# Performance work log

Hardware: AMD Instinct MI355X
Metric: run time of the kernel (lower is better)

## Reference

```python
import jax, jax.numpy as jnp
import numpy as np

DIM = 192; NH = 6; WS = 8; SS = 4
D_INNER = 384; D_STATE = 64; MNH = 6; HEADDIM = 64; DCONV = 4; CHUNK = 128


def layernorm(x, w, b):
    m = jnp.mean(x, axis=-1, keepdims=True)
    v = jnp.var(x, axis=-1, keepdims=True)
    return (x - m) * jax.lax.rsqrt(v + 1e-5) * w + b


def segsum(a):
    # a: (..., T) -> (..., T, T) with [i,j] = sum_{k=j+1..i} a_k (lower-tri), -inf-ish above diag
    T = a.shape[-1]
    x = jnp.broadcast_to(a[..., None], a.shape + (T,))
    lo = np.tril(np.ones((T, T), dtype=bool), -1)
    x = jnp.where(lo, x, 0.0)
    s = jnp.cumsum(x, axis=-2)
    keep = np.tril(np.ones((T, T), dtype=bool), 0)
    return jnp.where(keep, s, -1e9)


def ssd(X, a, Bm, Cm):
    # Mamba2 chunked state-space dual scan. X:(b,l,h,p) a:(b,l,h) Bm/Cm:(b,l,n)
    b, l, h, p = X.shape
    n = Bm.shape[-1]
    nc = l // CHUNK
    Xc = X.reshape(b, nc, CHUNK, h, p)
    ac = a.reshape(b, nc, CHUNK, h).transpose(0, 3, 1, 2)  # (b,h,c,cl)
    Bc = Bm.reshape(b, nc, CHUNK, n)
    Cc = Cm.reshape(b, nc, CHUNK, n)
    a_cs = jnp.cumsum(ac, axis=-1)
    Lm = jnp.exp(segsum(ac))  # (b,h,c,cl,cl)
    Y_diag = jnp.einsum('bcln,bcsn,bhcls,bcshp->bclhp', Cc, Bc, Lm, Xc)
    decay_states = jnp.exp(a_cs[..., -1:] - a_cs)
    states = jnp.einsum('bcln,bhcl,bclhp->bchpn', Bc, decay_states, Xc)
    a_last = jnp.pad(a_cs[..., -1], ((0, 0), (0, 0), (1, 0)))
    decay_chunk = jnp.exp(segsum(a_last))  # (b,h,c+1,c+1)
    states_cat = jnp.concatenate([jnp.zeros_like(states[:, :1]), states], axis=1)
    prev = jnp.einsum('bhzc,bchpn->bzhpn', decay_chunk, states_cat)[:, :-1]
    Y_off = jnp.einsum('bcln,bchpn,bhcl->bclhp', Cc, prev, jnp.exp(a_cs))
    return (Y_diag + Y_off).reshape(b, l, h, p)


def mamba2(xs, in_w, conv_w, conv_b, dt_bias, A_log, D, norm_w, out_w):
    b, l, _ = xs.shape
    zxbcdt = xs @ in_w.T  # (b,l,2*di+2*n+nh)
    z = zxbcdt[..., :D_INNER]
    xBC = zxbcdt[..., D_INNER:2 * D_INNER + 2 * D_STATE]
    dt = jax.nn.softplus(zxbcdt[..., -MNH:] + dt_bias)
    # causal depthwise conv1d
    xt = xBC.transpose(0, 2, 1)
    xt = jax.lax.conv_general_dilated(xt, conv_w[:, None, :], (1,), [(DCONV - 1, 0)],
                                      feature_group_count=xt.shape[1],
                                      dimension_numbers=('NCH', 'OIH', 'NCH'))
    xBC = jax.nn.silu((xt + conv_b[None, :, None]).transpose(0, 2, 1))
    xp = xBC[..., :D_INNER].reshape(b, l, MNH, HEADDIM)
    Bm = xBC[..., D_INNER:D_INNER + D_STATE]
    Cm = xBC[..., D_INNER + D_STATE:]
    A = -jnp.exp(A_log)
    y = ssd(xp * dt[..., None], dt * A, Bm, Cm)
    y = y + xp * D[None, None, :, None]
    y = y.reshape(b, l, D_INNER)
    y = y * jax.nn.silu(z)  # gated RMSNorm
    y = y * jax.lax.rsqrt(jnp.mean(y * y, axis=-1, keepdims=True) + 1e-5) * norm_w
    return y @ out_w.T


def build_mask(H, W):
    img = np.zeros((H, W))
    cnt = 0
    for hs in (slice(0, -WS), slice(-WS, -SS), slice(-SS, None)):
        for wsl in (slice(0, -WS), slice(-WS, -SS), slice(-SS, None)):
            img[hs, wsl] = cnt
            cnt += 1
    mw = img.reshape(H // WS, WS, W // WS, WS).transpose(0, 2, 1, 3).reshape(-1, WS * WS)
    diff = mw[:, None, :] - mw[:, :, None]
    return jnp.asarray(np.where(diff != 0, -100.0, 0.0).astype(np.float32))


def gated_window_attn(xw, mask, qkv_w, qkv_b, proj_w, proj_b, gate_w, gate_b):
    Bw, N, C = xw.shape
    hd = C // NH
    qkv = (xw @ qkv_w.T + qkv_b).reshape(Bw, N, 3, NH, hd).transpose(2, 0, 3, 1, 4)
    q, k, v = qkv[0], qkv[1], qkv[2]
    s = jnp.einsum('bhnd,bhmd->bhnm', q, k) * (hd ** -0.5)
    nW = mask.shape[0]
    s = (s.reshape(Bw // nW, nW, NH, N, N) + mask[None, :, None]).reshape(Bw, NH, N, N)
    a = jax.nn.softmax(s, axis=-1)
    o = jnp.einsum('bhnm,bhmd->bhnd', a, v).transpose(0, 2, 1, 3)  # (Bw,N,NH,hd)
    gate = jax.nn.sigmoid(xw @ gate_w.T + gate_b)  # per-head gate from pre-attn x
    o = (o * gate[..., None]).reshape(Bw, N, C)
    return o @ proj_w.T + proj_b


def lgs_forward(x, H, W, n1_w, n1_b, m_in_w, m_conv_w, m_conv_b, m_dt_bias, m_A_log,
                m_D, m_norm_w, m_out_w, qkv_w, qkv_b, proj_w, proj_b, gate_w, gate_b,
                fus_w, fus_b, eca_w, n2_w, n2_b, fc1_w, fc1_b, fc2_w, fc2_b):
    twoB, L, C = x.shape
    Bh = twoB // 2
    shortcut = x
    xn = layernorm(x, n1_w, n1_b)
    # Mamba branch: interleave frame0/frame1 tokens -> (Bh, 2L, C) scan -> de-interleave
    xs = jnp.stack([xn[:Bh], xn[Bh:]], axis=2).reshape(Bh, 2 * L, C)
    ym = mamba2(xs, m_in_w, m_conv_w, m_conv_b, m_dt_bias, m_A_log, m_D, m_norm_w, m_out_w)
    ym = ym.reshape(Bh, L, 2, C)
    x_mamba = jnp.concatenate([ym[:, :, 0], ym[:, :, 1]], axis=0)  # (2B,L,C)
    # shifted-window gated attention branch
    x2 = jnp.roll(xn.reshape(twoB, H, W, C), (-SS, -SS), axis=(1, 2))
    xw = x2.reshape(twoB, H // WS, WS, W // WS, WS, C).transpose(0, 1, 3, 2, 4, 5).reshape(-1, WS * WS, C)
    ow = gated_window_attn(xw, build_mask(H, W), qkv_w, qkv_b, proj_w, proj_b, gate_w, gate_b)
    ow = ow.reshape(twoB, H // WS, W // WS, WS, WS, C).transpose(0, 1, 3, 2, 4, 5).reshape(twoB, H, W, C)
    x_attn = jnp.roll(ow, (SS, SS), axis=(1, 2)).reshape(twoB, L, C)
    # fusion 1x1 conv == per-pixel linear over concatenated channels
    xf = jnp.concatenate([x_mamba, x_attn], axis=-1) @ fus_w.T + fus_b
    # ECAB: global-avg-pool channel attention via k=3 1D conv over channels
    pooled = jnp.pad(jnp.mean(xf, axis=1), ((0, 0), (1, 1)))
    ca = jax.nn.sigmoid(eca_w[0] * pooled[:, :-2] + eca_w[1] * pooled[:, 1:-1] + eca_w[2] * pooled[:, 2:])
    xf = xf * ca[:, None, :]
    xo = shortcut + xf
    h = layernorm(xo, n2_w, n2_b)
    h = jax.nn.gelu(h @ fc1_w.T + fc1_b, approximate=False) @ fc2_w.T + fc2_b
    return xo + h


def setup_inputs() -> dict:
    key = jax.random.key(0)
    ks = jax.random.split(key, 12)
    C = DIM

    def w(k, shape, s=0.02):
        return jax.random.normal(k, shape, jnp.float32) * s

    return {
        'x': jax.random.normal(ks[0], (4, 2304, C), jnp.float32),
        'H': 48, 'W': 48,
        'n1_w': jnp.ones((C,), jnp.float32), 'n1_b': jnp.zeros((C,), jnp.float32),
        'm_in_w': w(ks[1], (2 * D_INNER + 2 * D_STATE + MNH, C)),
        'm_conv_w': w(ks[2], (D_INNER + 2 * D_STATE, DCONV), 0.1),
        'm_conv_b': jnp.zeros((D_INNER + 2 * D_STATE,), jnp.float32),
        'm_dt_bias': jnp.log(jnp.expm1(jnp.full((MNH,), 0.01, jnp.float32))),
        'm_A_log': jnp.log(jnp.arange(1, MNH + 1, dtype=jnp.float32)),
        'm_D': jnp.ones((MNH,), jnp.float32),
        'm_norm_w': jnp.ones((D_INNER,), jnp.float32),
        'm_out_w': w(ks[3], (C, D_INNER)),
        'qkv_w': w(ks[4], (3 * C, C)), 'qkv_b': jnp.zeros((3 * C,), jnp.float32),
        'proj_w': w(ks[5], (C, C)), 'proj_b': jnp.zeros((C,), jnp.float32),
        'gate_w': w(ks[6], (NH, C)), 'gate_b': jnp.zeros((NH,), jnp.float32),
        'fus_w': w(ks[7], (C, 2 * C)), 'fus_b': jnp.zeros((C,), jnp.float32),
        'eca_w': w(ks[8], (3,), 0.3),
        'n2_w': jnp.ones((C,), jnp.float32), 'n2_b': jnp.zeros((C,), jnp.float32),
        'fc1_w': w(ks[9], (4 * C, C)), 'fc1_b': jnp.zeros((4 * C,), jnp.float32),
        'fc2_w': w(ks[10], (C, 4 * C)), 'fc2_b': jnp.zeros((C,), jnp.float32),
    }


def reference(x, H, W, n1_w, n1_b, m_in_w, m_conv_w, m_conv_b, m_dt_bias, m_A_log,
              m_D, m_norm_w, m_out_w, qkv_w, qkv_b, proj_w, proj_b, gate_w, gate_b,
              fus_w, fus_b, eca_w, n2_w, n2_b, fc1_w, fc1_b, fc2_w, fc2_b):
    return lgs_forward(x, H, W, n1_w, n1_b, m_in_w, m_conv_w, m_conv_b, m_dt_bias,
                       m_A_log, m_D, m_norm_w, m_out_w, qkv_w, qkv_b, proj_w, proj_b,
                       gate_w, gate_b, fus_w, fus_b, eca_w, n2_w, n2_b,
                       fc1_w, fc1_b, fc2_w, fc2_b)
```

## Files before the change

kernel.cpp:

```cpp
#include <hip/hip_runtime.h>
#include <math.h>

#define DEV __device__ __forceinline__

typedef __attribute__((ext_vector_type(8))) short short8;
typedef __attribute__((ext_vector_type(4))) float f32x4;

DEV float sigmoidf_(float x){ return 1.f/(1.f+__expf(-x)); }
DEV float siluf_(float x){ return x/(1.f+__expf(-x)); }
DEV float softplusf_(float x){ return (x>20.f)? x : log1pf(__expf(x)); }

DEV short bf16rne(float f){
  unsigned u=__float_as_uint(f);
  unsigned r=(u + 0x7FFFu + ((u>>16)&1u))>>16;
  return (short)r;
}
DEV unsigned short bf16u(float f){ return (unsigned short)bf16rne(f); }
DEV float b2f(unsigned short u){ return __uint_as_float(((unsigned)u)<<16); }
DEV float b2fs(short u){ return __uint_as_float(((unsigned)(unsigned short)u)<<16); }

DEV void gll16(const void* g, void* l){
  __builtin_amdgcn_global_load_lds(
      (const __attribute__((address_space(1))) void*)g,
      (__attribute__((address_space(3))) void*)(unsigned)(uintptr_t)l,
// ... 76 lines not shown
  #pragma unroll
  for(int p=0;p<NP;p++){
    if(p+1<NP) asm volatile("s_waitcnt vmcnt(4)":::"memory");
    else       asm volatile("s_waitcnt vmcnt(0)":::"memory");
    __builtin_amdgcn_s_barrier();
    compute(p,p&1);
    if(p+2<NP){
      __builtin_amdgcn_s_barrier();
      stage(p+2,p&1);
    }
  }

  __syncthreads();
  {
    int mbase=wid*16+4*kq;
    #pragma unroll
    for(int ni=0;ni<4;ni++)
      #pragma unroll
      for(int r=0;r<4;r++)
        sO[(mbase+r)*65 + ni*16+m16]=acc[ni][r];
  }
  __syncthreads();
  int erow=tid>>3, c0=(tid&7)*8;
  #pragma unroll
  for(int rd=0;rd<2;rd++){
    int ml=rd*32+erow;
    int m=bm+ml;
    int orow=map_row(m,smode);
    float v[8];
    #pragma unroll
    for(int j=0;j<8;j++) v[j]=sO[ml*65+c0+j];
    const float* rp=res? res+(size_t)orow*ldo+col_off : nullptr;
    #pragma unroll
    for(int j=0;j<8;j++){
      int nn=bn+c0+j;
      float val=v[j];
      if(bias && nn<N) val+=bias[nn];
      if(epi==2) val=0.5f*val*(1.f+erff(val*0.70710678118654752f));
      else if(epi==3) val+=rp[nn];
      v[j]=val;
    }
    size_t obase=(size_t)orow*ldo+col_off+bn+c0;
    if(bn+c0+7<N){
      if(Ob){
        short8 w;
        #pragma unroll
        for(int j=0;j<8;j++) w[j]=bf16rne(v[j]);
        *(short8*)(Ob+obase)=w;
      } else {
        float4 f0={v[0],v[1],v[2],v[3]}, f1={v[4],v[5],v[6],v[7]};
        *(float4*)(Of+obase)=f0;
        *(float4*)(Of+obase+4)=f1;
      }
    } else {
      #pragma unroll
      for(int j=0;j<8;j++){
        int nn=bn+c0+j;
        if(nn<N){ if(Ob) Ob[obase+j]=bf16rne(v[j]); else Of[obase+j]=v[j]; }
      }
    }
  }
  if(pool){
    if(tid<64){
      float s=0;
      #pragma unroll 8
      for(int ml=0;ml<64;ml++) s+=sO[ml*65+tid];
      if(bias) s+=64.f*bias[bn+tid];
      atomicAdd(&pool[(bm/2304)*192 + bn+tid], s);
    }
  }
}

template<int K>
__global__ __launch_bounds__(256,4) void k_gemm(const short* __restrict__ A, const short* __restrict__ W,
    const float* __restrict__ bias, const float* __restrict__ res,
    float* __restrict__ Of, short* __restrict__ Ob,
    int N, int ldo, int col_off, int gmode, int smode, int epi, float* __restrict__ pool){
  gemm_body<K>(A,W,bias,res,Of,Ob,N,ldo,col_off,gmode,smode,epi,blockIdx.x,blockIdx.y,pool);
}

__global__ __launch_bounds__(256,4) void k_gemm_inqkv(const short* __restrict__ xn,
    const short* __restrict__ w_in, short* __restrict__ zx,
    const short* __restrict__ w_qkv, const float* __restrict__ qkvb, short* __restrict__ qkv){
  if(blockIdx.y<15)
    gemm_body<192>(xn,w_in,nullptr,nullptr,nullptr,zx, 902,904,0, 1,0,0, blockIdx.x,blockIdx.y, nullptr);
  else
    gemm_body<192>(xn,w_qkv,qkvb,nullptr,nullptr,qkv, 576,576,0, 2,0,0, blockIdx.x,blockIdx.y-15, nullptr);
}

__global__ __launch_bounds__(256) void k_lnw2b(const float* __restrict__ in, const float* __restrict__ w,
    const float* __restrict__ b, short* __restrict__ out,
    const float* __restrict__ w0,const float* __restrict__ w1,const float* __restrict__ w2,
    const float* __restrict__ w3,const float* __restrict__ w4,const float* __restrict__ w5,
    const float* __restrict__ w6, short* __restrict__ dst){
  int bid=blockIdx.x;
  if(bid<2304){
    int warp=threadIdx.x>>6, lane=threadIdx.x&63;
    int row=bid*4+warp;
    const float* ip=in+(size_t)row*192;
    float v0=ip[lane], v1=ip[lane+64], v2=ip[lane+128];
    float s=v0+v1+v2, sq=v0*v0+v1*v1+v2*v2;
    #pragma unroll
    for(int off=32;off;off>>=1){ s+=__shfl_xor(s,off); sq+=__shfl_xor(sq,off); }
    float mean=s*(1.f/192.f), var=sq*(1.f/192.f)-mean*mean;
    float inv=rsqrtf(var+1e-5f);
    short* op=out+(size_t)row*192;
    op[lane]    =bf16rne((v0-mean)*inv*w[lane]    +b[lane]);
    op[lane+64] =bf16rne((v1-mean)*inv*w[lane+64] +b[lane+64]);
    op[lane+128]=bf16rne((v2-mean)*inv*w[lane+128]+b[lane+128]);
  } else {
    int flat=bid-2304;
    int seg=flat/677;
    int i=(flat-seg*677)*256+threadIdx.x;
    const float* src; int size, off;
    switch(seg){
      case 0: src=w0; size=173184; off=0;      break;
      case 1: src=w1; size=110592; off=173184; break;
      case 2: src=w2; size=73728;  off=283776; break;
      case 3: src=w3; size=36864;  off=357504; break;
      case 4: src=w4; size=73728;  off=394368; break;
      case 5: src=w5; size=147456; off=468096; break;
      default:src=w6; size=147456; off=615552; break;
    }
    if(i<size) dst[off+i]=bf16rne(src[i]);
  }
}

__global__ __launch_bounds__(256) void k_convprep(const short* __restrict__ zx, const float* __restrict__ cw,
    const float* __restrict__ cb, short* __restrict__ xbc,
    const float* __restrict__ dt_bias, const float* __restrict__ A_log,
    float* __restrict__ dtb, float* __restrict__ acs, float* __restrict__ csum){
  int bid=blockIdx.x;
  if(bid<2304){
    int idx=bid*256+threadIdx.x;
    int ch0=(idx&63)*8; int rl=idx>>6;
    int l=rl%4608;
    const short* base=zx+(size_t)rl*904+384+ch0;
    short8 x0=*(const short8*)(base);
    short8 x1={0,0,0,0,0,0,0,0},x2=x1,x3=x1;
    if(l>=1) x1=*(const short8*)(base-904);
    if(l>=2) x2=*(const short8*)(base-2*904);
    if(l>=3) x3=*(const short8*)(base-3*904);
    short8 out;
    #pragma unroll
    for(int j=0;j<8;j++){
      float4 w=*(const float4*)(cw+(ch0+j)*4);
      float acc=cb[ch0+j]
        + b2fs(x3[j])*w.x + b2fs(x2[j])*w.y + b2fs(x1[j])*w.z + b2fs(x0[j])*w.w;
      out[j]=bf16rne(siluf_(acc));
    }
    *(short8*)(xbc+(size_t)rl*512+ch0)=out;
  } else {
    int pb=bid-2304;
    int c=pb%36, h=(pb/36)%6, b=pb/216;
    int l=threadIdx.x;
    __shared__ float sb[128];
    float a=0.f;
    if(l<128){
      int row=b*4608+c*128+l;
      float xv=b2fs(zx[(size_t)row*904+896+h])+dt_bias[h];
      float dt=softplusf_(xv);
      a=-__expf(A_log[h])*dt;
      dtb[row*6+h]=dt;
      sb[l]=a;
    }
    __syncthreads();
    for(int off=1;off<128;off<<=1){
      float add=(l>=off && l<128)? sb[l-off]:0.f;
      __syncthreads();
      if(l<128) sb[l]+=add;
      __syncthreads();
    }
    if(l<128){
      acs[((size_t)(b*6+h)*36+c)*128+l]=sb[l];
      if(l==127) csum[(b*6+h)*36+c]=sb[127];
    }
  }
}

__global__ __launch_bounds__(256) void k_ssd_a(const short* __restrict__ xbc, const float* __restrict__ dtb,
    const float* __restrict__ acs, const float* __restrict__ csum,
    short* __restrict__ st, short* __restrict__ Y){
  int bid=blockIdx.x;
  int h=bid%6, c=(bid/6)%36, b=bid/216;
  __shared__ unsigned short sB[128][68];
  __shared__ unsigned short sC[128][68];
  __shared__ unsigned short sXdT[64][132];
  __shared__ unsigned short sBTE[64][132];
  __shared__ unsigned short sM[128][36];
  __shared__ float sAcs[128];
  __shared__ float sE[128];
  int tid=threadIdx.x;
  int lane=tid&63, wid=tid>>6;
  int m16=lane&15, kq=lane>>4;
  int base_row=b*4608+c*128;
  const float* acsp=acs+((size_t)(b*6+h)*36+c)*128;
  float tot=csum[(b*6+h)*36+c];
  if(tid<128){ float a=acsp[tid]; sAcs[tid]=a; sE[tid]=__expf(tot-a); }
  __syncthreads();
  for(int i=tid;i<1024;i+=256){
    int l=i>>3, n0=(i&7)*8;
    int row=base_row+l;
    const short* rp=xbc+(size_t)row*512;
    short8 Bv=*(const short8*)(rp+384+n0);
    short8 Cv=*(const short8*)(rp+448+n0);
    short8 Xv=*(const short8*)(rp+h*64+n0);
    float dt=dtb[row*6+h];
    float e=sE[l];
    *(short8*)&sB[l][n0]=Bv;
    *(short8*)&sC[l][n0]=Cv;
    #pragma unroll
    for(int j=0;j<8;j++){
      sXdT[n0+j][l]=bf16u(b2fs(Xv[j])*dt);
      sBTE[n0+j][l]=bf16u(b2fs(Bv[j])*e);
    }
  }
  __syncthreads();
  {
    int wr=wid>>1, wc=wid&1;
    f32x4 accS[2][2];
    #pragma unroll
    for(int mi=0;mi<2;mi++)
      #pragma unroll
      for(int ni=0;ni<2;ni++) accS[mi][ni]=(f32x4){0.f,0.f,0.f,0.f};
    #pragma unroll
    for(int ks=0;ks<4;ks++){
      short8 a0=*(const short8*)&sXdT[wr*32+m16][ks*32+kq*8];
      short8 a1=*(const short8*)&sXdT[wr*32+16+m16][ks*32+kq*8];
      short8 b0=*(const short8*)&sBTE[wc*32+m16][ks*32+kq*8];
      short8 b1=*(const short8*)&sBTE[wc*32+16+m16][ks*32+kq*8];
      accS[0][0]=__builtin_amdgcn_mfma_f32_16x16x32_bf16(a0,b0,accS[0][0],0,0,0);
      accS[0][1]=__builtin_amdgcn_mfma_f32_16x16x32_bf16(a0,b1,accS[0][1],0,0,0);
      accS[1][0]=__builtin_amdgcn_mfma_f32_16x16x32_bf16(a1,b0,accS[1][0],0,0,0);
      accS[1][1]=__builtin_amdgcn_mfma_f32_16x16x32_bf16(a1,b1,accS[1][1],0,0,0);
    }
    short* op=st+((size_t)((b*36+c)*6+h))*4096;
    #pragma unroll
    for(int mi=0;mi<2;mi++)
      #pragma unroll
      for(int ni=0;ni<2;ni++)
        #pragma unroll
        for(int r=0;r<4;r++){
          int p=wr*32+mi*16+4*kq+r, n=wc*32+ni*16+m16;
          op[p*64+n]=bf16rne(accS[mi][ni][r]);
        }
  }
  #pragma unroll
  for(int ti=0;ti<2;ti++){
    int t = ti? (7-wid) : wid;
    f32x4 accY[4];
    #pragma unroll
    for(int pi=0;pi<4;pi++) accY[pi]=(f32x4){0.f,0.f,0.f,0.f};
    int nslab=(t>>1)+1;
    for(int jt=0;jt<nslab;jt++){
      f32x4 accD[2];
      accD[0]=(f32x4){0.f,0.f,0.f,0.f}; accD[1]=(f32x4){0.f,0.f,0.f,0.f};
      #pragma unroll
      for(int ks=0;ks<2;ks++){
        short8 a =*(const short8*)&sC[t*16+m16][ks*32+kq*8];
        short8 b0=*(const short8*)&sB[jt*32+m16][ks*32+kq*8];
        short8 b1=*(const short8*)&sB[jt*32+16+m16][ks*32+kq*8];
        accD[0]=__builtin_amdgcn_mfma_f32_16x16x32_bf16(a,b0,accD[0],0,0,0);
        accD[1]=__builtin_amdgcn_mfma_f32_16x16x32_bf16(a,b1,accD[1],0,0,0);
      }
      int lrow=t*16+4*kq;
      #pragma unroll
      for(int sti=0;sti<2;sti++)
        #pragma unroll
        for(int r=0;r<4;r++){
          int l=lrow+r, s=jt*32+sti*16+m16;
          float v=(s<=l)? __expf(sAcs[l]-sAcs[s])*accD[sti][r] : 0.f;
          sM[l][sti*16+m16]=bf16u(v);
        }
      short8 am=*(const short8*)&sM[t*16+m16][kq*8];
      #pragma unroll
      for(int pi=0;pi<4;pi++){
        short8 bx=*(const short8*)&sXdT[pi*16+m16][jt*32+kq*8];
        accY[pi]=__builtin_amdgcn_mfma_f32_16x16x32_bf16(am,bx,accY[pi],0,0,0);
      }
    }
    #pragma unroll
    for(int pi=0;pi<4;pi++)
      #pragma unroll
      for(int r=0;r<4;r++){
        int l=t*16+4*kq+r, p=pi*16+m16;
        Y[(size_t)(base_row+l)*384+h*64+p]=bf16rne(accY[pi][r]);
      }
  }
}

__global__ __launch_bounds__(256) void k_scan(const short* __restrict__ st, const float* __restrict__ csum,
                                              short* __restrict__ prevb){
  int bid=blockIdx.x;
  int seg=bid&15, bh=bid>>4;
  int b=bh/6, h=bh%6;
  __shared__ float sE[36];
  if(threadIdx.x<36) sE[threadIdx.x]=__expf(csum[(b*6+h)*36+threadIdx.x]);
  __syncthreads();
  int e=seg*256+threadIdx.x;
  size_t stride=(size_t)6*4096;
  size_t idx=((size_t)((b*36+0)*6+h))*4096+e;
  float carry=0.f;
  for(int c4=0;c4<36;c4+=4){
    float v[4];
    #pragma unroll
    for(int j=0;j<4;j++) v[j]=b2fs(st[idx+j*stride]);
    #pragma unroll
    for(int j=0;j<4;j++){
      prevb[idx+j*stride]=bf16rne(carry);
      carry=carry*sE[c4+j]+v[j];
    }
    idx+=4*stride;
  }
}

__global__ __launch_bounds__(256) void k_ssd_b(const short* __restrict__ xbc, const short* __restrict__ prevb,
    const float* __restrict__ acs, const float* __restrict__ Dv, short* __restrict__ Y){
  int bid=blockIdx.x;
  int h=bid%6, c=(bid/6)%36, b=bid/216;
  __shared__ unsigned short sC[128][68];
  __shared__ unsigned short sP[64][68];
  __shared__ float sAcs[128];
  int tid=threadIdx.x;
  int lane=tid&63, wid=tid>>6;
  int m16=lane&15, kq=lane>>4;
  int base_row=b*4608+c*128;
  const float* acsp=acs+((size_t)(b*6+h)*36+c)*128;
  if(tid<128) sAcs[tid]=acsp[tid];
  for(int i=tid;i<1024;i+=256){
    int l=i>>3, n0=(i&7)*8;
    short8 Cv=*(const short8*)(xbc+(size_t)(base_row+l)*512+448+n0);
    *(short8*)&sC[l][n0]=Cv;
  }
  const short* pp=prevb+((size_t)((b*36+c)*6+h))*4096;
  for(int i=tid;i<512;i+=256){
    int p_=i>>3, n0=(i&7)*8;
    short8 Pv=*(const short8*)(pp+p_*64+n0);
    *(short8*)&sP[p_][n0]=Pv;
  }
  __syncthreads();
  float Dh=Dv[h];
  int lt0=2*wid;
  f32x4 acc[2][4];
  #pragma unroll
  for(int li=0;li<2;li++)
    #pragma unroll
    for(int pi=0;pi<4;pi++) acc[li][pi]=(f32x4){0.f,0.f,0.f,0.f};
  #pragma unroll
  for(int ks=0;ks<2;ks++){
    short8 a0=*(const short8*)&sC[lt0*16+m16][ks*32+kq*8];
    short8 a1=*(const short8*)&sC[(lt0+1)*16+m16][ks*32+kq*8];
    #pragma unroll
    for(int pi=0;pi<4;pi++){
      short8 bp=*(const short8*)&sP[pi*16+m16][ks*32+kq*8];
      acc[0][pi]=__builtin_amdgcn_mfma_f32_16x16x32_bf16(a0,bp,acc[0][pi],0,0,0);
      acc[1][pi]=__builtin_amdgcn_mfma_f32_16x16x32_bf16(a1,bp,acc[1][pi],0,0,0);
    }
  }
  #pragma unroll
  for(int li=0;li<2;li++){
    #pragma unroll
    for(int r=0;r<4;r++){
      int l=(lt0+li)*16+4*kq+r;
      int row=base_row+l;
      float e=__expf(sAcs[l]);
      #pragma unroll
      for(int pi=0;pi<4;pi++){
        int p=pi*16+m16;
        size_t yi=(size_t)row*384+h*64+p;
        float xpv=b2fs(xbc[(size_t)row*512+h*64+p]);
        Y[yi]=bf16rne(b2fs(Y[yi])+acc[li][pi][r]*e+xpv*Dh);
      }
    }
  }
}

__global__ __launch_bounds__(256) void k_rmsgate(const short* __restrict__ Y, const short* __restrict__ zx,
    const float* __restrict__ nw, short* __restrict__ yn, float* __restrict__ partial){
  if(blockIdx.x<3){
    int t=blockIdx.x*256+threadIdx.x;
    if(t<768) partial[t]=0.f;
  }
  int warp=threadIdx.x>>6, lane=threadIdx.x&63;
  int row=blockIdx.x*4+warp;
  float v[6]; float ss=0.f;
  #pragma unroll
  for(int j=0;j<6;j++){
    int cidx=lane+64*j;
    float y=b2fs(Y[(size_t)row*384+cidx]);
    float z=b2fs(zx[(size_t)row*904+cidx]);
    y*=siluf_(z);
    v[j]=y; ss+=y*y;
  }
  #pragma unroll
  for(int off=32;off;off>>=1) ss+=__shfl_xor(ss,off);
  float sc=rsqrtf(ss*(1.f/384.f)+1e-5f);
  #pragma unroll
  for(int j=0;j<6;j++){
    int cidx=lane+64*j;
    yn[(size_t)row*384+cidx]=bf16rne(v[j]*sc*nw[cidx]);
  }
}

__global__ __launch_bounds__(128) void k_att2(const short* __restrict__ qkv, const short* __restrict__ xn,
    const float* __restrict__ gw, const float* __restrict__ gb, short* __restrict__ obuf){
  int bid=blockIdx.x;
  int widx=bid/6, head=bid-widx*6;
  int b=widx/36, t=widx-b*36;
  int wi=t/6, wj=t-wi*6;
  int n=threadIdx.x&63, half=threadIdx.x>>6;
  __shared__ float sK[64][32], sV[64][32];
  __shared__ float sO2[64][32];
  __shared__ float sM2[64], sD2[64];
  const short* qp=qkv+(size_t)(widx*64+n)*576+head*32;
  float q[32];
  {
    short8 v0=*(const short8*)(qp),    v1=*(const short8*)(qp+8);
    short8 v2=*(const short8*)(qp+16), v3=*(const short8*)(qp+24);
    #pragma unroll
    for(int i=0;i<8;i++){ q[i]=b2fs(v0[i]); q[8+i]=b2fs(v1[i]); q[16+i]=b2fs(v2[i]); q[24+i]=b2fs(v3[i]); }
    short8 k0=*(const short8*)(qp+192+half*16), k1=*(const short8*)(qp+200+half*16);
    short8 u0=*(const short8*)(qp+384+half*16), u1=*(const short8*)(qp+392+half*16);
    #pragma unroll
    for(int i=0;i<8;i++){
      sK[n][half*16+i]=b2fs(k0[i]); sK[n][half*16+8+i]=b2fs(k1[i]);
      sV[n][half*16+i]=b2fs(u0[i]); sV[n][half*16+8+i]=b2fs(u1[i]);
    }
  }
  int h2=wi*8+(n>>3), w2=wj*8+(n&7);
  int rh=(h2<40)?0:((h2<44)?1:2);
  int rw=(w2<40)?0:((w2<44)?1:2);
  int myid=rh*3+rw;
  __syncthreads();
  const float scale=0.17677669529663687f;
  float p[32]; float mx=-1e30f;
  #pragma unroll 4
  for(int jj=0;jj<32;jj++){
    int j=half*32+jj;
    float sc=0;
    #pragma unroll
    for(int d=0;d<32;d++) sc+=q[d]*sK[j][d];
    int hj=wi*8+(j>>3), wjj=wj*8+(j&7);
    int rhj=(hj<40)?0:((hj<44)?1:2);
    int rwj=(wjj<40)?0:((wjj<44)?1:2);
    float m=((rhj*3+rwj)!=myid)? -100.f:0.f;
    float v=sc*scale+m;
    p[jj]=v; mx=fmaxf(mx,v);
  }
  float den=0;
  #pragma unroll
  for(int jj=0;jj<32;jj++){ p[jj]=__expf(p[jj]-mx); den+=p[jj]; }
  float o[32];
  #pragma unroll
  for(int d=0;d<32;d++) o[d]=0.f;
  #pragma unroll 4
  for(int jj=0;jj<32;jj++){
    float pj=p[jj];
    #pragma unroll
    for(int d=0;d<32;d++) o[d]+=pj*sV[half*32+jj][d];
  }
  if(half==1){
    sM2[n]=mx; sD2[n]=den;
    #pragma unroll
    for(int d=0;d<32;d++) sO2[n][d]=o[d];
  }
  __syncthreads();
  if(half==0){
    float m1=sM2[n], d1=sD2[n];
    float m=fmaxf(mx,m1);
    float e0=__expf(mx-m), e1=__expf(m1-m);
    float dent=den*e0+d1*e1;
    int xrow=map_row(widx*64+n,2);
    const short* xp=xn+(size_t)xrow*192;
    const float* gwp=gw+head*192;
    float g=0;
    #pragma unroll
    for(int c=0;c<24;c++){
      short8 xv=*(const short8*)(xp+c*8);
      float4 w0=*(const float4*)(gwp+c*8);
      float4 w1=*(const float4*)(gwp+c*8+4);
      g+=b2fs(xv[0])*w0.x+b2fs(xv[1])*w0.y+b2fs(xv[2])*w0.z+b2fs(xv[3])*w0.w
        +b2fs(xv[4])*w1.x+b2fs(xv[5])*w1.y+b2fs(xv[6])*w1.z+b2fs(xv[7])*w1.w;
    }
    g=sigmoidf_(g+gb[head]);
    float fac=g/dent;
    short* op=obuf+(size_t)(widx*64+n)*192+head*32;
    #pragma unroll
    for(int v8=0;v8<4;v8++){
      short8 w;
      #pragma unroll
      for(int j=0;j<8;j++){
        int d=v8*8+j;
        w[j]=bf16rne((o[d]*e0+sO2[n][d]*e1)*fac);
      }
      *(short8*)(op+v8*8)=w;
    }
  }
}

__global__ __launch_bounds__(768) void k_ca(const float* __restrict__ partial, const float* __restrict__ ecaw,
                                            float* __restrict__ ca){
  int tid=threadIdx.x;
  int cidx=tid%192;
  float pv=partial[tid]*(1.f/2304.f);
  __shared__ float sP[768];
  sP[tid]=pv; __syncthreads();
  float left =(cidx>0)?   sP[tid-1]:0.f;
  float right=(cidx<191)? sP[tid+1]:0.f;
  ca[tid]=sigmoidf_(ecaw[0]*left+ecaw[1]*pv+ecaw[2]*right);
}

__global__ __launch_bounds__(256) void k_xoln(const float* __restrict__ x, const float* __restrict__ xf,
    const float* __restrict__ ca, const float* __restrict__ w, const float* __restrict__ bvec,
    float* __restrict__ xo, short* __restrict__ out){
  int warp=threadIdx.x>>6, lane=threadIdx.x&63;
  int row=blockIdx.x*4+warp;
  int bidx=row/2304;
  const float* cap=ca+bidx*192;
  const float* xp=x+(size_t)row*192;
  const float* fp=xf+(size_t)row*192;
  float v0=xp[lane]    +fp[lane]    *cap[lane];
  float v1=xp[lane+64] +fp[lane+64] *cap[lane+64];
  float v2=xp[lane+128]+fp[lane+128]*cap[lane+128];
  float* op=xo+(size_t)row*192;
  op[lane]=v0; op[lane+64]=v1; op[lane+128]=v2;
  float s=v0+v1+v2, sq=v0*v0+v1*v1+v2*v2;
  #pragma unroll
  for(int off=32;off;off>>=1){ s+=__shfl_xor(s,off); sq+=__shfl_xor(sq,off); }
  float mean=s*(1.f/192.f), var=sq*(1.f/192.f)-mean*mean;
  float inv=rsqrtf(var+1e-5f);
  short* bp=out+(size_t)row*192;
  bp[lane]    =bf16rne((v0-mean)*inv*w[lane]    +bvec[lane]);
  bp[lane+64] =bf16rne((v1-mean)*inv*w[lane+64] +bvec[lane+64]);
  bp[lane+128]=bf16rne((v2-mean)*inv*w[lane+128]+bvec[lane+128]);
}

extern "C" void kernel_launch(void* const* d_in, const int* in_sizes, int n_in,
                              void* d_out, int out_size, void* d_ws, size_t ws_size,
                              hipStream_t stream){
  const float* x     =(const float*)d_in[0];
  const float* n1w   =(const float*)d_in[3];
  const float* n1b   =(const float*)d_in[4];
  const float* m_in_w=(const float*)d_in[5];
  const float* m_cw  =(const float*)d_in[6];
  const float* m_cb  =(const float*)d_in[7];
  const float* m_dtb =(const float*)d_in[8];
  const float* m_Al  =(const float*)d_in[9];
  const float* m_D   =(const float*)d_in[10];
  const float* m_nw  =(const float*)d_in[11];
  const float* m_ow  =(const float*)d_in[12];
  const float* qkvw  =(const float*)d_in[13];
  const float* qkvb  =(const float*)d_in[14];
  const float* projw =(const float*)d_in[15];
  const float* projb =(const float*)d_in[16];
  const float* gatew =(const float*)d_in[17];
  const float* gateb =(const float*)d_in[18];
  const float* fusw  =(const float*)d_in[19];
  const float* fusb  =(const float*)d_in[20];
  const float* ecaw  =(const float*)d_in[21];
  const float* n2w   =(const float*)d_in[22];
  const float* n2b   =(const float*)d_in[23];
  const float* fc1w  =(const float*)d_in[24];
  const float* fc1b  =(const float*)d_in[25];
  const float* fc2w  =(const float*)d_in[26];
  const float* fc2b  =(const float*)d_in[27];
  float* out=(float*)d_out;
  float* ws=(float*)d_ws;

  short* xn_bf  = (short*)(ws + 0);
  short* wb     = (short*)(ws + 884736);
  short* zx_bf  = (short*)(ws + 1266240);
  short* xbc_bf = (short*)(ws + 5431872);
  float* dtb    = ws + 7791168;
  float* acs    = ws + 7846464;
  float* csum   = ws + 7901760;
  short* st_bf  = (short*)(ws + 7902272);
  short* prevb_bf=(short*)(ws + 9671744);
  short* Y_bf   = (short*)(ws + 11441216);
  float* bigbf  = ws + 14980160;
  short* qkv_bf = (short*)(ws + 18519104);
  short* hbuf_bf= xn_bf;
  short* obuf_bf= xbc_bf;
  short* xcat_bf= prevb_bf;
  float* xf     = (float*)st_bf;
  float* xo     = (float*)Y_bf;
  short* yn_bf  = (short*)bigbf;
  short* h1_bf  = (short*)bigbf;
  float* partial= dtb;
  float* ca     = acs;
  short* wb_in  = wb + 0;
  short* wb_qkv = wb + 173184;
  short* wb_out = wb + 283776;
  short* wb_proj= wb + 357504;
  short* wb_fus = wb + 394368;
  short* wb_fc1 = wb + 468096;
  short* wb_fc2 = wb + 615552;

  k_lnw2b<<<7043,256,0,stream>>>(x,n1w,n1b,xn_bf, m_in_w,qkvw,m_ow,projw,fusw,fc1w,fc2w,wb);
  k_gemm_inqkv<<<dim3(144,24),256,0,stream>>>(xn_bf,wb_in,zx_bf,wb_qkv,qkvb,qkv_bf);
  k_convprep<<<2736,256,0,stream>>>(zx_bf,m_cw,m_cb,xbc_bf, m_dtb,m_Al,dtb,acs,csum);
  k_ssd_a<<<432,256,0,stream>>>(xbc_bf,dtb,acs,csum,st_bf,Y_bf);
  k_scan<<<192,256,0,stream>>>(st_bf,csum,prevb_bf);
  k_ssd_b<<<432,256,0,stream>>>(xbc_bf,prevb_bf,acs,m_D,Y_bf);
  k_rmsgate<<<2304,256,0,stream>>>(Y_bf,zx_bf,m_nw,yn_bf,partial);
  k_gemm<384><<<dim3(144,3),256,0,stream>>>(yn_bf,wb_out,nullptr,nullptr,nullptr,xcat_bf, 192,384,0, 0,1,0, nullptr);
  k_att2<<<864,128,0,stream>>>(qkv_bf,xn_bf,gatew,gateb,obuf_bf);
  k_gemm<192><<<dim3(144,3),256,0,stream>>>(obuf_bf,wb_proj,projb,nullptr,nullptr,xcat_bf, 192,384,192, 0,2,0, nullptr);
  k_gemm<384><<<dim3(144,3),256,0,stream>>>(xcat_bf,wb_fus,fusb,nullptr,xf,nullptr, 192,192,0, 0,0,0, partial);
  k_ca<<<1,768,0,stream>>>(partial,ecaw,ca);
  k_xoln<<<2304,256,0,stream>>>(x,xf,ca,n2w,n2b,xo,hbuf_bf);
  k_gemm<192><<<dim3(144,12),256,0,stream>>>(hbuf_bf,wb_fc1,fc1b,nullptr,nullptr,h1_bf, 768,768,0, 0,0,2, nullptr);
  k_gemm<768><<<dim3(144,3),256,0,stream>>>(h1_bf,wb_fc2,fc2b,xo,out,nullptr, 192,192,0, 0,0,3, nullptr);
}
```

Measured before the change: 170.7 us.

## Fuse window attention into SSD chunk kernel and fold channel attention into xoln

The window attention kernel becomes extra blocks of the SSD intra-chunk kernel, with a shared-memory union and two attention heads packed per 256-thread block. This lets the two independent stages run concurrently in one launch instead of in separate launches. The tiny single-block channel-attention kernel is removed and its sigmoid/conv is recomputed inline in the xoln kernel. The attention output gets its own workspace buffer so it no longer aliases the SSD input it now runs alongside. The costs are a larger union shared-memory footprint for the attention blocks and redundant per-row recomputation of the ECA gate.

After: 182.4 us. 6.9% more time.

```diff
diff --git a/kernel.cpp b/kernel.cpp
--- a/kernel.cpp
+++ b/kernel.cpp
@@ -182,10 +182,11 @@
 __global__ __launch_bounds__(256,4) void k_gemm_inqkv(const short* __restrict__ xn,
     const short* __restrict__ w_in, short* __restrict__ zx,
     const short* __restrict__ w_qkv, const float* __restrict__ qkvb, short* __restrict__ qkv){
-  if(blockIdx.y<15)
-    gemm_body<192>(xn,w_in,nullptr,nullptr,nullptr,zx, 902,904,0, 1,0,0, blockIdx.x,blockIdx.y, nullptr);
-  else
-    gemm_body<192>(xn,w_qkv,qkvb,nullptr,nullptr,qkv, 576,576,0, 2,0,0, blockIdx.x,blockIdx.y-15, nullptr);
+  int by=blockIdx.y;
+  const short* W; short* O; const float* bias; int N,ldo,gm,byy;
+  if(by<15){ W=w_in;  O=zx;  bias=nullptr; N=902; ldo=904; gm=1; byy=by; }
+  else     { W=w_qkv; O=qkv; bias=qkvb;    N=576; ldo=576; gm=2; byy=by-15; }
+  gemm_body<192>(xn,W,bias,nullptr,nullptr,O, N,ldo,0, gm,0,0, blockIdx.x,byy, nullptr);
 }
 
 __global__ __launch_bounds__(256) void k_lnw2b(const float* __restrict__ in, const float* __restrict__ w,
@@ -255,14 +256,12 @@
     int c=pb%36, h=(pb/36)%6, b=pb/216;
     int l=threadIdx.x;
     __shared__ float sb[128];
-    float a=0.f;
     if(l<128){
       int row=b*4608+c*128+l;
       float xv=b2fs(zx[(size_t)row*904+896+h])+dt_bias[h];
       float dt=softplusf_(xv);
-      a=-__expf(A_log[h])*dt;
       dtb[row*6+h]=dt;
-      sb[l]=a;
+      sb[l]=-__expf(A_log[h])*dt;
     }
     __syncthreads();
     for(int off=1;off<128;off<<=1){
@@ -278,114 +277,221 @@
   }
 }
 
-__global__ __launch_bounds__(256) void k_ssd_a(const short* __restrict__ xbc, const float* __restrict__ dtb,
+struct SsdS {
+  unsigned short sB[128][68];
+  unsigned short sC[128][68];
+  unsigned short sXdT[64][132];
+  unsigned short sBTE[64][132];
+  unsigned short sM[128][36];
+  float sAcs[128];
+  float sE[128];
+};
+struct AttS {
+  float sK[2][64][32];
+  float sV[2][64][32];
+  float sO2[2][64][32];
+  float sM2[2][64];
+  float sD2[2][64];
+};
+
+__global__ __launch_bounds__(256) void k_ssd_att(const short* __restrict__ xbc, const float* __restrict__ dtb,
     const float* __restrict__ acs, const float* __restrict__ csum,
-    short* __restrict__ st, short* __restrict__ Y){
-  int bid=blockIdx.x;
-  int h=bid%6, c=(bid/6)%36, b=bid/216;
-  __shared__ unsigned short sB[128][68];
-  __shared__ unsigned short sC[128][68];
-  __shared__ unsigned short sXdT[64][132];
-  __shared__ unsigned short sBTE[64][132];
-  __shared__ unsigned short sM[128][36];
-  __shared__ float sAcs[128];
-  __shared__ float sE[128];
+    short* __restrict__ st, short* __restrict__ Y,
+    const short* __restrict__ qkv, const short* __restrict__ xn,
+    const float* __restrict__ gw, const float* __restrict__ gb, short* __restrict__ obuf){
+  __shared__ union { SsdS s; AttS a; } u;
   int tid=threadIdx.x;
-  int lane=tid&63, wid=tid>>6;
-  int m16=lane&15, kq=lane>>4;
-  int base_row=b*4608+c*128;
-  const float* acsp=acs+((size_t)(b*6+h)*36+c)*128;
-  float tot=csum[(b*6+h)*36+c];
-  if(tid<128){ float a=acsp[tid]; sAcs[tid]=a; sE[tid]=__expf(tot-a); }
-  __syncthreads();
-  for(int i=tid;i<1024;i+=256){
-    int l=i>>3, n0=(i&7)*8;
-    int row=base_row+l;
-    const short* rp=xbc+(size_t)row*512;
-    short8 Bv=*(const short8*)(rp+384+n0);
-    short8 Cv=*(const short8*)(rp+448+n0);
-    short8 Xv=*(const short8*)(rp+h*64+n0);
-    float dt=dtb[row*6+h];
-    float e=sE[l];
-    *(short8*)&sB[l][n0]=Bv;
-    *(short8*)&sC[l][n0]=Cv;
-    #pragma unroll
-    for(int j=0;j<8;j++){
-      sXdT[n0+j][l]=bf16u(b2fs(Xv[j])*dt);
-      sBTE[n0+j][l]=bf16u(b2fs(Bv[j])*e);
-    }
-  }
-  __syncthreads();
-  {
-    int wr=wid>>1, wc=wid&1;
-    f32x4 accS[2][2];
-    #pragma unroll
-    for(int mi=0;mi<2;mi++)
-      #pragma unroll
-      for(int ni=0;ni<2;ni++) accS[mi][ni]=(f32x4){0.f,0.f,0.f,0.f};
-    #pragma unroll
-    for(int ks=0;ks<4;ks++){
-      short8 a0=*(const short8*)&sXdT[wr*32+m16][ks*32+kq*8];
-      short8 a1=*(const short8*)&sXdT[wr*32+16+m16][ks*32+kq*8];
-      short8 b0=*(const short8*)&sBTE[wc*32+m16][ks*32+kq*8];
-      short8 b1=*(const short8*)&sBTE[wc*32+16+m16][ks*32+kq*8];
-      accS[0][0]=__builtin_amdgcn_mfma_f32_16x16x32_bf16(a0,b0,accS[0][0],0,0,0);
-      accS[0][1]=__builtin_amdgcn_mfma_f32_16x16x32_bf16(a0,b1,accS[0][1],0,0,0);
-      accS[1][0]=__builtin_amdgcn_mfma_f32_16x16x32_bf16(a1,b0,accS[1][0],0,0,0);
-      accS[1][1]=__builtin_amdgcn_mfma_f32_16x16x32_bf16(a1,b1,accS[1][1],0,0,0);
-    }
-    short* op=st+((size_t)((b*36+c)*6+h))*4096;
-    #pragma unroll
-    for(int mi=0;mi<2;mi++)
-      #pragma unroll
-      for(int ni=0;ni<2;ni++)
+  if(blockIdx.x<432){
+    int bid=blockIdx.x;
+    int h=bid%6, c=(bid/6)%36, b=bid/216;
+    int lane=tid&63, wid=tid>>6;
+    int m16=lane&15, kq=lane>>4;
+    int base_row=b*4608+c*128;
+    const float* acsp=acs+((size_t)(b*6+h)*36+c)*128;
+    float tot=csum[(b*6+h)*36+c];
+    if(tid<128){ float a=acsp[tid]; u.s.sAcs[tid]=a; u.s.sE[tid]=__expf(tot-a); }
+    __syncthreads();
+    for(int i=tid;i<1024;i+=256){
+      int l=i>>3, n0=(i&7)*8;
+      int row=base_row+l;
+      const short* rp=xbc+(size_t)row*512;
+      short8 Bv=*(const short8*)(rp+384+n0);
+      short8 Cv=*(const short8*)(rp+448+n0);
+      short8 Xv=*(const short8*)(rp+h*64+n0);
+      float dt=dtb[row*6+h];
+      float e=u.s.sE[l];
+      *(short8*)&u.s.sB[l][n0]=Bv;
+      *(short8*)&u.s.sC[l][n0]=Cv;
+      #pragma unroll
+      for(int j=0;j<8;j++){
+        u.s.sXdT[n0+j][l]=bf16u(b2fs(Xv[j])*dt);
+        u.s.sBTE[n0+j][l]=bf16u(b2fs(Bv[j])*e);
+      }
+    }
+    __syncthreads();
+    {
+      int wr=wid>>1, wc=wid&1;
+      f32x4 accS[2][2];
+      #pragma unroll
+      for(int mi=0;mi<2;mi++)
+        #pragma unroll
+        for(int ni=0;ni<2;ni++) accS[mi][ni]=(f32x4){0.f,0.f,0.f,0.f};
+      #pragma unroll
+      for(int ks=0;ks<4;ks++){
+        short8 a0=*(const short8*)&u.s.sXdT[wr*32+m16][ks*32+kq*8];
+        short8 a1=*(const short8*)&u.s.sXdT[wr*32+16+m16][ks*32+kq*8];
+        short8 b0=*(const short8*)&u.s.sBTE[wc*32+m16][ks*32+kq*8];
+        short8 b1=*(const short8*)&u.s.sBTE[wc*32+16+m16][ks*32+kq*8];
+        accS[0][0]=__builtin_amdgcn_mfma_f32_16x16x32_bf16(a0,b0,accS[0][0],0,0,0);
+        accS[0][1]=__builtin_amdgcn_mfma_f32_16x16x32_bf16(a0,b1,accS[0][1],0,0,0);
+        accS[1][0]=__builtin_amdgcn_mfma_f32_16x16x32_bf16(a1,b0,accS[1][0],0,0,0);
+        accS[1][1]=__builtin_amdgcn_mfma_f32_16x16x32_bf16(a1,b1,accS[1][1],0,0,0);
+      }
+      short* op=st+((size_t)((b*36+c)*6+h))*4096;
+      #pragma unroll
+      for(int mi=0;mi<2;mi++)
+        #pragma unroll
+        for(int ni=0;ni<2;ni++)
+          #pragma unroll
+          for(int r=0;r<4;r++){
+            int p=wr*32+mi*16+4*kq+r, n=wc*32+ni*16+m16;
+            op[p*64+n]=bf16rne(accS[mi][ni][r]);
+          }
+    }
+    #pragma unroll
+    for(int ti=0;ti<2;ti++){
+      int t = ti? (7-wid) : wid;
+      f32x4 accY[4];
+      #pragma unroll
+      for(int pi=0;pi<4;pi++) accY[pi]=(f32x4){0.f,0.f,0.f,0.f};
+      int nslab=(t>>1)+1;
+      for(int jt=0;jt<nslab;jt++){
+        f32x4 accD[2];
+        accD[0]=(f32x4){0.f,0.f,0.f,0.f}; accD[1]=(f32x4){0.f,0.f,0.f,0.f};
+        #pragma unroll
+        for(int ks=0;ks<2;ks++){
+          short8 a =*(const short8*)&u.s.sC[t*16+m16][ks*32+kq*8];
+          short8 b0=*(const short8*)&u.s.sB[jt*32+m16][ks*32+kq*8];
+          short8 b1=*(const short8*)&u.s.sB[jt*32+16+m16][ks*32+kq*8];
+          accD[0]=__builtin_amdgcn_mfma_f32_16x16x32_bf16(a,b0,accD[0],0,0,0);
+          accD[1]=__builtin_amdgcn_mfma_f32_16x16x32_bf16(a,b1,accD[1],0,0,0);
+        }
+        int lrow=t*16+4*kq;
+        #pragma unroll
+        for(int sti=0;sti<2;sti++)
+          #pragma unroll
+          for(int r=0;r<4;r++){
+            int l=lrow+r, s=jt*32+sti*16+m16;
+            float v=(s<=l)? __expf(u.s.sAcs[l]-u.s.sAcs[s])*accD[sti][r] : 0.f;
+            u.s.sM[l][sti*16+m16]=bf16u(v);
+          }
+        short8 am=*(const short8*)&u.s.sM[t*16+m16][kq*8];
+        #pragma unroll
+        for(int pi=0;pi<4;pi++){
+          short8 bx=*(const short8*)&u.s.sXdT[pi*16+m16][jt*32+kq*8];
+          accY[pi]=__builtin_amdgcn_mfma_f32_16x16x32_bf16(am,bx,accY[pi],0,0,0);
+        }
+      }
+      #pragma unroll
+      for(int pi=0;pi<4;pi++)
         #pragma unroll
         for(int r=0;r<4;r++){
-          int p=wr*32+mi*16+4*kq+r, n=wc*32+ni*16+m16;
-          op[p*64+n]=bf16rne(accS[mi][ni][r]);
+          int l=t*16+4*kq+r, p=pi*16+m16;
+          Y[(size_t)(base_row+l)*384+h*64+p]=bf16rne(accY[pi][r]);
         }
-  }
-  #pragma unroll
-  for(int ti=0;ti<2;ti++){
-    int t = ti? (7-wid) : wid;
-    f32x4 accY[4];
-    #pragma unroll
-    for(int pi=0;pi<4;pi++) accY[pi]=(f32x4){0.f,0.f,0.f,0.f};
-    int nslab=(t>>1)+1;
-    for(int jt=0;jt<nslab;jt++){
-      f32x4 accD[2];
-      accD[0]=(f32x4){0.f,0.f,0.f,0.f}; accD[1]=(f32x4){0.f,0.f,0.f,0.f};
-      #pragma unroll
-      for(int ks=0;ks<2;ks++){
-        short8 a =*(const short8*)&sC[t*16+m16][ks*32+kq*8];
-        short8 b0=*(const short8*)&sB[jt*32+m16][ks*32+kq*8];
-        short8 b1=*(const short8*)&sB[jt*32+16+m16][ks*32+kq*8];
-        accD[0]=__builtin_amdgcn_mfma_f32_16x16x32_bf16(a,b0,accD[0],0,0,0);
-        accD[1]=__builtin_amdgcn_mfma_f32_16x16x32_bf16(a,b1,accD[1],0,0,0);
-      }
-      int lrow=t*16+4*kq;
-      #pragma unroll
-      for(int sti=0;sti<2;sti++)
+    }
+  } else {
+    int pair=tid>>7;
+    int t2=tid&127;
+    int n=t2&63, half=t2>>6;
+    int abid=(blockIdx.x-432)*2+pair;
+    int widx=abid/6, head=abid-widx*6;
+    int b=widx/36, t=widx-b*36;
+    int wi=t/6, wj=t-wi*6;
+    const short* qp=qkv+(size_t)(widx*64+n)*576+head*32;
+    float q[32];
+    {
+      short8 v0=*(const short8*)(qp),    v1=*(const short8*)(qp+8);
+      short8 v2=*(const short8*)(qp+16), v3=*(const short8*)(qp+24);
+      #pragma unroll
+      for(int i=0;i<8;i++){ q[i]=b2fs(v0[i]); q[8+i]=b2fs(v1[i]); q[16+i]=b2fs(v2[i]); q[24+i]=b2fs(v3[i]); }
+      short8 k0=*(const short8*)(qp+192+half*16), k1=*(const short8*)(qp+200+half*16);
+      short8 u0=*(const short8*)(qp+384+half*16), u1=*(const short8*)(qp+392+half*16);
+      #pragma unroll
+      for(int i=0;i<8;i++){
+        u.a.sK[pair][n][half*16+i]=b2fs(k0[i]); u.a.sK[pair][n][half*16+8+i]=b2fs(k1[i]);
+        u.a.sV[pair][n][half*16+i]=b2fs(u0[i]); u.a.sV[pair][n][half*16+8+i]=b2fs(u1[i]);
+      }
+    }
+    int h2=wi*8+(n>>3), w2=wj*8+(n&7);
+    int rh=(h2<40)?0:((h2<44)?1:2);
+    int rw=(w2<40)?0:((w2<44)?1:2);
+    int myid=rh*3+rw;
+    __syncthreads();
+    const float scale=0.17677669529663687f;
+    float p[32]; float mx=-1e30f;
+    #pragma unroll 4
+    for(int jj=0;jj<32;jj++){
+      int j=half*32+jj;
+      float sc=0;
+      #pragma unroll
+      for(int d=0;d<32;d++) sc+=q[d]*u.a.sK[pair][j][d];
+      int hj=wi*8+(j>>3), wjj=wj*8+(j&7);
+      int rhj=(hj<40)?0:((hj<44)?1:2);
+      int rwj=(wjj<40)?0:((wjj<44)?1:2);
+      float m=((rhj*3+rwj)!=myid)? -100.f:0.f;
+      float v=sc*scale+m;
+      p[jj]=v; mx=fmaxf(mx,v);
+    }
+    float den=0;
+    #pragma unroll
+    for(int jj=0;jj<32;jj++){ p[jj]=__expf(p[jj]-mx); den+=p[jj]; }
+    float o[32];
+    #pragma unroll
+    for(int d=0;d<32;d++) o[d]=0.f;
+    #pragma unroll 4
+    for(int jj=0;jj<32;jj++){
+      float pj=p[jj];
+      #pragma unroll
+      for(int d=0;d<32;d++) o[d]+=pj*u.a.sV[pair][half*32+jj][d];
+    }
+    if(half==1){
+      u.a.sM2[pair][n]=mx; u.a.sD2[pair][n]=den;
+      #pragma unroll
+      for(int d=0;d<32;d++) u.a.sO2[pair][n][d]=o[d];
+    }
+    __syncthreads();
+    if(half==0){
+      float m1=u.a.sM2[pair][n], d1=u.a.sD2[pair][n];
+      float m=fmaxf(mx,m1);
+      float e0=__expf(mx-m), e1=__expf(m1-m);
+      float dent=den*e0+d1*e1;
+      int xrow=map_row(widx*64+n,2);
+      const short* xp=xn+(size_t)xrow*192;
+      const float* gwp=gw+head*192;
+      float g=0;
+      #pragma unroll
+      for(int c=0;c<24;c++){
+        short8 xv=*(const short8*)(xp+c*8);
+        float4 w0=*(const float4*)(gwp+c*8);
+        float4 w1=*(const float4*)(gwp+c*8+4);
+        g+=b2fs(xv[0])*w0.x+b2fs(xv[1])*w0.y+b2fs(xv[2])*w0.z+b2fs(xv[3])*w0.w
+          +b2fs(xv[4])*w1.x+b2fs(xv[5])*w1.y+b2fs(xv[6])*w1.z+b2fs(xv[7])*w1.w;
+      }
+      g=sigmoidf_(g+gb[head]);
+      float fac=g/dent;
+      short* op=obuf+(size_t)(widx*64+n)*192+head*32;
+      #pragma unroll
+      for(int v8=0;v8<4;v8++){
+        short8 w;
         #pragma unroll
-        for(int r=0;r<4;r++){
-          int l=lrow+r, s=jt*32+sti*16+m16;
-          float v=(s<=l)? __expf(sAcs[l]-sAcs[s])*accD[sti][r] : 0.f;
-          sM[l][sti*16+m16]=bf16u(v);
+        for(int j=0;j<8;j++){
+          int d=v8*8+j;
+          w[j]=bf16rne((o[d]*e0+u.a.sO2[pair][n][d]*e1)*fac);
         }
-      short8 am=*(const short8*)&sM[t*16+m16][kq*8];
-      #pragma unroll
-      for(int pi=0;pi<4;pi++){
-        short8 bx=*(const short8*)&sXdT[pi*16+m16][jt*32+kq*8];
-        accY[pi]=__builtin_amdgcn_mfma_f32_16x16x32_bf16(am,bx,accY[pi],0,0,0);
-      }
-    }
-    #pragma unroll
-    for(int pi=0;pi<4;pi++)
-      #pragma unroll
-      for(int r=0;r<4;r++){
-        int l=t*16+4*kq+r, p=pi*16+m16;
-        Y[(size_t)(base_row+l)*384+h*64+p]=bf16rne(accY[pi][r]);
-      }
+        *(short8*)(op+v8*8)=w;
+      }
+    }
   }
 }
 
@@ -502,126 +608,26 @@
   }
 }
 
-__global__ __launch_bounds__(128) void k_att2(const short* __restrict__ qkv, const short* __restrict__ xn,
-    const float* __restrict__ gw, const float* __restrict__ gb, short* __restrict__ obuf){
-  int bid=blockIdx.x;
-  int widx=bid/6, head=bid-widx*6;
-  int b=widx/36, t=widx-b*36;
-  int wi=t/6, wj=t-wi*6;
-  int n=threadIdx.x&63, half=threadIdx.x>>6;
-  __shared__ float sK[64][32], sV[64][32];
-  __shared__ float sO2[64][32];
-  __shared__ float sM2[64], sD2[64];
-  const short* qp=qkv+(size_t)(widx*64+n)*576+head*32;
-  float q[32];
-  {
-    short8 v0=*(const short8*)(qp),    v1=*(const short8*)(qp+8);
-    short8 v2=*(const short8*)(qp+16), v3=*(const short8*)(qp+24);
-    #pragma unroll
-    for(int i=0;i<8;i++){ q[i]=b2fs(v0[i]); q[8+i]=b2fs(v1[i]); q[16+i]=b2fs(v2[i]); q[24+i]=b2fs(v3[i]); }
-    short8 k0=*(const short8*)(qp+192+half*16), k1=*(const short8*)(qp+200+half*16);
-    short8 u0=*(const short8*)(qp+384+half*16), u1=*(const short8*)(qp+392+half*16);
-    #pragma unroll
-    for(int i=0;i<8;i++){
-      sK[n][half*16+i]=b2fs(k0[i]); sK[n][half*16+8+i]=b2fs(k1[i]);
-      sV[n][half*16+i]=b2fs(u0[i]); sV[n][half*16+8+i]=b2fs(u1[i]);
-    }
-  }
-  int h2=wi*8+(n>>3), w2=wj*8+(n&7);
-  int rh=(h2<40)?0:((h2<44)?1:2);
-  int rw=(w2<40)?0:((w2<44)?1:2);
-  int myid=rh*3+rw;
-  __syncthreads();
-  const float scale=0.17677669529663687f;
-  float p[32]; float mx=-1e30f;
-  #pragma unroll 4
-  for(int jj=0;jj<32;jj++){
-    int j=half*32+jj;
-    float sc=0;
-    #pragma unroll
-    for(int d=0;d<32;d++) sc+=q[d]*sK[j][d];
-    int hj=wi*8+(j>>3), wjj=wj*8+(j&7);
-    int rhj=(hj<40)?0:((hj<44)?1:2);
-    int rwj=(wjj<40)?0:((wjj<44)?1:2);
-    float m=((rhj*3+rwj)!=myid)? -100.f:0.f;
-    float v=sc*scale+m;
-    p[jj]=v; mx=fmaxf(mx,v);
-  }
-  float den=0;
-  #pragma unroll
-  for(int jj=0;jj<32;jj++){ p[jj]=__expf(p[jj]-mx); den+=p[jj]; }
-  float o[32];
-  #pragma unroll
-  for(int d=0;d<32;d++) o[d]=0.f;
-  #pragma unroll 4
-  for(int jj=0;jj<32;jj++){
-    float pj=p[jj];
-    #pragma unroll
-    for(int d=0;d<32;d++) o[d]+=pj*sV[half*32+jj][d];
-  }
-  if(half==1){
-    sM2[n]=mx; sD2[n]=den;
-    #pragma unroll
-    for(int d=0;d<32;d++) sO2[n][d]=o[d];
-  }
-  __syncthreads();
-  if(half==0){
-    float m1=sM2[n], d1=sD2[n];
-    float m=fmaxf(mx,m1);
-    float e0=__expf(mx-m), e1=__expf(m1-m);
-    float dent=den*e0+d1*e1;
-    int xrow=map_row(widx*64+n,2);
-    const short* xp=xn+(size_t)xrow*192;
-    const float* gwp=gw+head*192;
-    float g=0;
-    #pragma unroll
-    for(int c=0;c<24;c++){
-      short8 xv=*(const short8*)(xp+c*8);
-      float4 w0=*(const float4*)(gwp+c*8);
-      float4 w1=*(const float4*)(gwp+c*8+4);
-      g+=b2fs(xv[0])*w0.x+b2fs(xv[1])*w0.y+b2fs(xv[2])*w0.z+b2fs(xv[3])*w0.w
-        +b2fs(xv[4])*w1.x+b2fs(xv[5])*w1.y+b2fs(xv[6])*w1.z+b2fs(xv[7])*w1.w;
-    }
-    g=sigmoidf_(g+gb[head]);
-    float fac=g/dent;
-    short* op=obuf+(size_t)(widx*64+n)*192+head*32;
-    #pragma unroll
-    for(int v8=0;v8<4;v8++){
-      short8 w;
-      #pragma unroll
-      for(int j=0;j<8;j++){
-        int d=v8*8+j;
-        w[j]=bf16rne((o[d]*e0+sO2[n][d]*e1)*fac);
-      }
-      *(short8*)(op+v8*8)=w;
-    }
-  }
-}
-
-__global__ __launch_bounds__(768) void k_ca(const float* __restrict__ partial, const float* __restrict__ ecaw,
-                                            float* __restrict__ ca){
-  int tid=threadIdx.x;
-  int cidx=tid%192;
-  float pv=partial[tid]*(1.f/2304.f);
-  __shared__ float sP[768];
-  sP[tid]=pv; __syncthreads();
-  float left =(cidx>0)?   sP[tid-1]:0.f;
-  float right=(cidx<191)? sP[tid+1]:0.f;
-  ca[tid]=sigmoidf_(ecaw[0]*left+ecaw[1]*pv+ecaw[2]*right);
-}
-
 __global__ __launch_bounds__(256) void k_xoln(const float* __restrict__ x, const float* __restrict__ xf,
-    const float* __restrict__ ca, const float* __restrict__ w, const float* __restrict__ bvec,
+    const float* __restrict__ partial, const float* __restrict__ ecaw,
+    const float* __restrict__ w, const float* __restrict__ bvec,
     float* __restrict__ xo, short* __restrict__ out){
   int warp=threadIdx.x>>6, lane=threadIdx.x&63;
   int row=blockIdx.x*4+warp;
   int bidx=row/2304;
-  const float* cap=ca+bidx*192;
+  const float* pp=partial+bidx*192;
+  float e0=ecaw[0], e1=ecaw[1], e2=ecaw[2];
+  auto cav=[&](int c)->float{
+    float pv=pp[c];
+    float lft=(c>0)?   pp[c-1]:0.f;
+    float rgt=(c<191)? pp[c+1]:0.f;
+    return sigmoidf_((e0*lft+e1*pv+e2*rgt)*(1.f/2304.f));
+  };
   const float* xp=x+(size_t)row*192;
   const float* fp=xf+(size_t)row*192;
-  float v0=xp[lane]    +fp[lane]    *cap[lane];
-  float v1=xp[lane+64] +fp[lane+64] *cap[lane+64];
-  float v2=xp[lane+128]+fp[lane+128]*cap[lane+128];
+  float v0=xp[lane]    +fp[lane]    *cav(lane);
+  float v1=xp[lane+64] +fp[lane+64] *cav(lane+64);
+  float v2=xp[lane+128]+fp[lane+128]*cav(lane+128);
   float* op=xo+(size_t)row*192;
   op[lane]=v0; op[lane+64]=v1; op[lane+128]=v2;
   float s=v0+v1+v2, sq=v0*v0+v1*v1+v2*v2;
@@ -679,15 +685,14 @@
   short* Y_bf   = (short*)(ws + 11441216);
   float* bigbf  = ws + 14980160;
   short* qkv_bf = (short*)(ws + 18519104);
+  short* obuf_bf= (short*)(ws + 21173312);
   short* hbuf_bf= xn_bf;
-  short* obuf_bf= xbc_bf;
   short* xcat_bf= prevb_bf;
   float* xf     = (float*)st_bf;
   float* xo     = (float*)Y_bf;
   short* yn_bf  = (short*)bigbf;
   short* h1_bf  = (short*)bigbf;
   float* partial= dtb;
-  float* ca     = acs;
   short* wb_in  = wb + 0;
   short* wb_qkv = wb + 173184;
   short* wb_out = wb + 283776;
@@ -699,16 +704,14 @@
   k_lnw2b<<<7043,256,0,stream>>>(x,n1w,n1b,xn_bf, m_in_w,qkvw,m_ow,projw,fusw,fc1w,fc2w,wb);
   k_gemm_inqkv<<<dim3(144,24),256,0,stream>>>(xn_bf,wb_in,zx_bf,wb_qkv,qkvb,qkv_bf);
   k_convprep<<<2736,256,0,stream>>>(zx_bf,m_cw,m_cb,xbc_bf, m_dtb,m_Al,dtb,acs,csum);
-  k_ssd_a<<<432,256,0,stream>>>(xbc_bf,dtb,acs,csum,st_bf,Y_bf);
+  k_ssd_att<<<864,256,0,stream>>>(xbc_bf,dtb,acs,csum,st_bf,Y_bf, qkv_bf,xn_bf,gatew,gateb,obuf_bf);
   k_scan<<<192,256,0,stream>>>(st_bf,csum,prevb_bf);
   k_ssd_b<<<432,256,0,stream>>>(xbc_bf,prevb_bf,acs,m_D,Y_bf);
   k_rmsgate<<<2304,256,0,stream>>>(Y_bf,zx_bf,m_nw,yn_bf,partial);
   k_gemm<384><<<dim3(144,3),256,0,stream>>>(yn_bf,wb_out,nullptr,nullptr,nullptr,xcat_bf, 192,384,0, 0,1,0, nullptr);
-  k_att2<<<864,128,0,stream>>>(qkv_bf,xn_bf,gatew,gateb,obuf_bf);
   k_gemm<192><<<dim3(144,3),256,0,stream>>>(obuf_bf,wb_proj,projb,nullptr,nullptr,xcat_bf, 192,384,192, 0,2,0, nullptr);
   k_gemm<384><<<dim3(144,3),256,0,stream>>>(xcat_bf,wb_fus,fusb,nullptr,xf,nullptr, 192,192,0, 0,0,0, partial);
-  k_ca<<<1,768,0,stream>>>(partial,ecaw,ca);
-  k_xoln<<<2304,256,0,stream>>>(x,xf,ca,n2w,n2b,xo,hbuf_bf);
+  k_xoln<<<2304,256,0,stream>>>(x,xf,partial,ecaw,n2w,n2b,xo,hbuf_bf);
   k_gemm<192><<<dim3(144,12),256,0,stream>>>(hbuf_bf,wb_fc1,fc1b,nullptr,nullptr,h1_bf, 768,768,0, 0,0,2, nullptr);
   k_gemm<768><<<dim3(144,3),256,0,stream>>>(h1_bf,wb_fc2,fc2b,xo,out,nullptr, 192,192,0, 0,0,3, nullptr);
 }
```
